# Optimization experiments

Measured on AMD Instinct MI355X. Metric: run time of the kernel, lower is better.

The kernel has to match this reference:

```python
import jax, jax.numpy as jnp
import numpy as np

# --- static module config (from init_kwargs) ---
C1_OUT = 64          # c1OutChannels
C1K = 400            # k winners in conv layer
N_FC = 1024          # fc1 hidden units (n)
K_FC = 100           # k winners in fc1
BOOST = 1.0          # boostStrength
W_SPARSITY = 0.5     # weightSparsity: fraction of fc1 weights allowed nonzero
HP = 12              # pooled spatial size: floor((28-5+1)/2)
C1_OUTPUT_LEN = C1_OUT * HP * HP  # 9216
BATCH = 4096


def setup_inputs() -> dict:
    key = jax.random.key(0)
    ks = jax.random.split(key, 10)
    x = jax.random.normal(ks[0], (BATCH, 1, 28, 28), jnp.float32)
    c1_w = jax.random.normal(ks[1], (C1_OUT, 1, 5, 5), jnp.float32) * 0.1
    c1_b = jax.random.normal(ks[2], (C1_OUT,), jnp.float32) * 0.01
    # duty cycles live in [0, ~density]
    duty_cnn = jax.random.uniform(ks[3], (1, C1_OUT, 1, 1), jnp.float32) * 0.05
    fc1_w = jax.random.normal(ks[4], (N_FC, C1_OUT_LEN_ := C1_OUTPUT_LEN), jnp.float32) * 0.01
    fc1_mask_raw = jax.random.uniform(ks[5], (N_FC, C1_OUTPUT_LEN), jnp.float32)
    fc1_b = jax.random.normal(ks[6], (N_FC,), jnp.float32) * 0.01
    duty_fc = jax.random.uniform(ks[7], (N_FC,), jnp.float32) * 0.1
    fc2_w = jax.random.normal(ks[8], (10, N_FC), jnp.float32) * 0.05
    fc2_b = jnp.zeros((10,), jnp.float32)
    return dict(x=x, c1_w=c1_w, c1_b=c1_b, duty_cnn=duty_cnn, fc1_w=fc1_w,
                fc1_mask_raw=fc1_mask_raw, fc1_b=fc1_b, duty_fc=duty_fc,
                fc2_w=fc2_w, fc2_b=fc2_b)


def _kwinners(x_flat, boost_flat, k):
    """Duty-cycle-boosted k-winner mask.
    x_flat: [B, N]; boost_flat: [1, N] broadcastable boost factors.
    Keeps original x values at the top-k boosted positions per row, zeros rest.
    Boosting uses stop_gradient(x), matching KWinners*.forward(x.detach()*boost).
    """
    boosted = jax.lax.stop_gradient(x_flat) * boost_flat
    thr = jax.lax.top_k(boosted, k)[0][:, -1:]  # k-th largest per row
    return jnp.where(boosted >= thr, x_flat, jnp.zeros((), x_flat.dtype))


def reference(x, c1_w, c1_b, duty_cnn, fc1_w, fc1_mask_raw, fc1_b, duty_fc,
              fc2_w, fc2_b):
    B = x.shape[0]
    # conv2d (valid, stride 1) -> [B, 64, 24, 24]
    y = jax.lax.conv_general_dilated(
        x, c1_w, window_strides=(1, 1), padding='VALID',
        dimension_numbers=('NCHW', 'OIHW', 'NCHW')) + c1_b[None, :, None, None]
    # max_pool2d(2) -> [B, 64, 12, 12]
    y = jax.lax.reduce_window(y, -jnp.inf, jax.lax.max,
                              (1, 1, 2, 2), (1, 1, 2, 2), 'VALID')
    # KWinnersCNN: global top-k over flattened (C,H,W), per-channel boost
    target_density = C1K / C1_OUTPUT_LEN
    boost_c = jnp.exp((target_density - duty_cnn) * BOOST)  # [1,C,1,1]
    boost_flat = jnp.broadcast_to(boost_c, (1, C1_OUT, HP, HP)).reshape(1, -1)
    yf = _kwinners(y.reshape(B, -1), boost_flat, C1K)  # [B, 9216]
    # LinearSDR fc1: sparse-weight linear + KWinners
    w_mask = (fc1_mask_raw < W_SPARSITY).astype(fc1_w.dtype)
    h = yf @ (fc1_w * w_mask).T + fc1_b  # [B, 1024]
    boost_fc = jnp.exp((K_FC / N_FC - duty_fc) * BOOST)[None, :]
    h = _kwinners(h, boost_fc, K_FC)
    # fc2 + log_softmax (dropout inactive in eval mode)
    logits = h @ fc2_w.T + fc2_b
    return jax.nn.log_softmax(logits, axis=1)
```

## Files before the change

kernel.cpp:

```cpp
#include <hip/hip_runtime.h>

__device__ __forceinline__ float b2f(unsigned short u) {
  return __uint_as_float(((unsigned)u) << 16);
}
__device__ __forceinline__ unsigned short f2b(float f) {
  unsigned u = __float_as_uint(f);
  return (unsigned short)((u + 0x7FFFu + ((u >> 16) & 1u)) >> 16);
}
__device__ __forceinline__ float gload(const void* p, int i, int isb) {
  return isb ? b2f(((const unsigned short*)p)[i]) : ((const float*)p)[i];
}
__device__ __forceinline__ unsigned tokey(float f) {
  unsigned u = __float_as_uint(f);
  return u ^ (unsigned)(((int)u >> 31) | 0x80000000u);
}

__global__ void k_detect(const void* x, int* flag) {
  int tid = threadIdx.x;
  unsigned short u = ((const unsigned short*)x)[2 * tid];
  int e = (u >> 7) & 0xFF;
  bool sane = (e >= 100 && e <= 140);
  unsigned long long m = __ballot(sane);
  if (tid == 0) *flag = (__popcll(m) >= 40) ? 1 : 0;
}

__global__ __launch_bounds__(256) void k_prep(const void* __restrict__ fc1w,
                                              const void* __restrict__ mraw,
                                              float* __restrict__ WtF,
                                              const int* __restrict__ flag) {
  __shared__ float tile[64][65];
  const int isb = *flag;
  const int i0 = blockIdx.x * 64;
  const int u0 = blockIdx.y * 64;
  const int tx = threadIdx.x & 63, ty = threadIdx.x >> 6;
  for (int uu = ty; uu < 64; uu += 4) {
    int gi = (u0 + uu) * 9216 + i0 + tx;
    float wv = gload(fc1w, gi, isb);
    float mv = gload(mraw, gi, isb);
    tile[uu][tx] = (mv < 0.5f) ? wv : 0.0f;
  }
  __syncthreads();
  for (int ii = ty; ii < 64; ii += 4)
    WtF[(i0 + ii) * 1024 + u0 + tx] = tile[tx][ii];
}

__global__ __launch_bounds__(256) void k_conv(const void* __restrict__ x,
                                              const void* __restrict__ c1w_g,
                                              const void* __restrict__ c1b_g,
                                              const void* __restrict__ duty_g,
                                              int2* __restrict__ wpair,
                                              int* __restrict__ wcnt,
                                              const int* __restrict__ flag) {
  __shared__ __align__(16) float img[784];
  __shared__ float cw[1600];
  __shared__ float cb[64], bcs[64];
  __shared__ __align__(16) float pooled[9216];
  __shared__ unsigned hist[256];
  __shared__ unsigned selb, selk;
  const int tid = threadIdx.x;
  const int b = blockIdx.x;
  const int isb = *flag;

  for (int i = tid; i < 784; i += 256) img[i] = gload(x, b * 784 + i, isb);
  for (int i = tid; i < 1600; i += 256) cw[i] = gload(c1w_g, i, isb);
  if (tid < 64) {
    cb[tid] = gload(c1b_g, tid, isb);
    float arg = (float)(400.0 / 9216.0) - gload(duty_g, tid, isb);
    bcs[tid] = (float)exp((double)arg);
  }
  __syncthreads();

  for (int s = 0; s < 6; ++s) {
    int t = tid + (s << 8);
    int c = t / 24;
    int sub = t - c * 24;
    int ph = sub >> 1;
    int half = sub & 1;
    float w[25];
#pragma unroll
    for (int i = 0; i < 25; ++i) w[i] = cw[c * 25 + i];
    float R[6][16];
#pragma unroll
    for (int rr = 0; rr < 6; ++rr) {
      int row = 2 * ph + rr;
#pragma unroll
      for (int q = 0; q < 4; ++q)
        ((float4*)&R[rr][0])[q] = ((const float4*)img)[row * 7 + half * 3 + q];
    }
    float a0[12], a1[12];
#pragma unroll
    for (int j = 0; j < 12; ++j) { a0[j] = 0.f; a1[j] = 0.f; }
#pragma unroll
    for (int kj = 0; kj < 5; ++kj) {
#pragma unroll
      for (int kr = 0; kr < 5; ++kr) {
        float wk = w[kr * 5 + kj];
#pragma unroll
        for (int j = 0; j < 12; ++j) {
          a0[j] = fmaf(R[kr][j + kj], wk, a0[j]);
          a1[j] = fmaf(R[kr + 1][j + kj], wk, a1[j]);
        }
      }
    }
    float bias = cb[c];
    int obase = c * 144 + ph * 12 + half * 6;
#pragma unroll
    for (int q = 0; q < 6; ++q) {
      float m = fmaxf(fmaxf(a0[2 * q], a0[2 * q + 1]),
                      fmaxf(a1[2 * q], a1[2 * q + 1]));
      pooled[obase + q] = m + bias;
    }
  }
  __syncthreads();

  unsigned kfix = 0;
  int kk = 400;
  for (int pass = 3; pass >= 0; --pass) {
    const int shift = pass * 8;
    const unsigned himask = (pass == 3) ? 0u : (0xFFFFFFFFu << (shift + 8));
    hist[tid] = 0;
    __syncthreads();
    for (int e = 0; e < 9; ++e) {
      float4 pv = ((float4*)pooled)[tid * 9 + e];
#pragma unroll
      for (int q = 0; q < 4; ++q) {
        int o = tid * 36 + e * 4 + q;
        unsigned key = tokey(((float*)&pv)[q] * bcs[o / 144]);
        if (((key ^ kfix) & himask) == 0)
          atomicAdd(&hist[(key >> shift) & 255u], 1u);
      }
    }
    __syncthreads();
    unsigned v = hist[tid];
    for (int offs = 1; offs < 256; offs <<= 1) {
      unsigned other = (tid + offs < 256) ? hist[tid + offs] : 0u;
      __syncthreads();
      v += other;
      hist[tid] = v;
      __syncthreads();
    }
    unsigned snext = (tid < 255) ? hist[tid + 1] : 0u;
    if (v >= (unsigned)kk && snext < (unsigned)kk) {
      selb = (unsigned)tid;
      selk = (unsigned)(kk - (int)snext);
    }
    __syncthreads();
    kfix |= selb << shift;
    kk = (int)selk;
    __syncthreads();
  }

  int mycnt = 0;
#pragma unroll
  for (int e = 0; e < 36; ++e) {
    int o = tid * 36 + e;
    if (tokey(pooled[o] * bcs[o / 144]) >= kfix) ++mycnt;
  }
  hist[tid] = (unsigned)mycnt;
  __syncthreads();
  unsigned v2 = hist[tid];
  for (int offs = 1; offs < 256; offs <<= 1) {
    unsigned other = (tid >= offs) ? hist[tid - offs] : 0u;
    __syncthreads();
    v2 += other;
    hist[tid] = v2;
    __syncthreads();
  }
  int pos = (int)v2 - mycnt;
  for (int e = 0; e < 36; ++e) {
    int o = tid * 36 + e;
    float pv = pooled[o];
    if (tokey(pv * bcs[o / 144]) >= kfix) {
      if (pos < 512) wpair[b * 512 + pos] = make_int2(__float_as_int(pv), o);
      ++pos;
    }
  }
  if (tid == 255) wcnt[b] = (int)(v2 < 512u ? v2 : 512u);
}

__global__ __launch_bounds__(128) void k_fc1(const float* __restrict__ WtF,
                                             const int2* __restrict__ wpair,
                                             const int* __restrict__ wcnt,
                                             const void* __restrict__ fc1b,
                                             float* __restrict__ h,
                                             const int* __restrict__ flag) {
  __shared__ float sval[512];
  __shared__ int sidx[512];
  const int tid = threadIdx.x;
  const int img = blockIdx.x >> 3;
  const int slice = blockIdx.x & 7;
  const int isb = *flag;
  const int cnt = wcnt[img];
  for (int i = tid; i < cnt; i += 128) {
    int2 p = wpair[img * 512 + i];
    sval[i] = __int_as_float(p.x);
    sidx[i] = p.y;
  }
  __syncthreads();
  const int u = (slice << 7) | tid;
  const float* W = WtF + u;
  float acc = 0.f;
  for (int w = 0; w < cnt; ++w)
    acc = fmaf(sval[w], W[sidx[w] * 1024], acc);
  h[img * 1024 + u] = acc + gload(fc1b, u, isb);
}

__global__ __launch_bounds__(256) void k_sel(const float* __restrict__ h,
                                             const void* __restrict__ dutyfc,
                                             const void* __restrict__ fc2w,
                                             const void* __restrict__ fc2b,
                                             void* __restrict__ out,
                                             const int* __restrict__ flag) {
  __shared__ unsigned hist[256];
  __shared__ unsigned selb, selk;
  __shared__ double lg[10];
  __shared__ double mred[2];
  const int tid = threadIdx.x;
  const int row = blockIdx.x;
  const int isb = *flag;
  if (tid < 10) lg[tid] = (double)gload(fc2b, tid, isb);
  __syncthreads();

  const int u0 = 2 * tid, u1 = 2 * tid + 1, u2 = 512 + 2 * tid, u3 = 513 + 2 * tid;
  float2 hlo = ((const float2*)(h + row * 1024))[tid];
  float2 hhi = ((const float2*)(h + row * 1024 + 512))[tid];
  float h0 = hlo.x, h1 = hlo.y, h2 = hhi.x, h3 = hhi.y;
  float bf0 = (float)exp((double)(0.09765625f - gload(dutyfc, u0, isb)));
  float bf1 = (float)exp((double)(0.09765625f - gload(dutyfc, u1, isb)));
  float bf2 = (float)exp((double)(0.09765625f - gload(dutyfc, u2, isb)));
  float bf3 = (float)exp((double)(0.09765625f - gload(dutyfc, u3, isb)));
  unsigned k0 = tokey(h0 * bf0);
  unsigned k1 = tokey(h1 * bf1);
  unsigned k2 = tokey(h2 * bf2);
  unsigned k3 = tokey(h3 * bf3);

  unsigned kfix = 0;
  int kk = 100;
  for (int pass = 3; pass >= 0; --pass) {
    const int shift = pass * 8;
    const unsigned himask = (pass == 3) ? 0u : (0xFFFFFFFFu << (shift + 8));
    hist[tid] = 0;
    __syncthreads();
    if (((k0 ^ kfix) & himask) == 0) atomicAdd(&hist[(k0 >> shift) & 255u], 1u);
    if (((k1 ^ kfix) & himask) == 0) atomicAdd(&hist[(k1 >> shift) & 255u], 1u);
    if (((k2 ^ kfix) & himask) == 0) atomicAdd(&hist[(k2 >> shift) & 255u], 1u);
    if (((k3 ^ kfix) & himask) == 0) atomicAdd(&hist[(k3 >> shift) & 255u], 1u);
    __syncthreads();
    unsigned v = hist[tid];
    for (int offs = 1; offs < 256; offs <<= 1) {
      unsigned other = (tid + offs < 256) ? hist[tid + offs] : 0u;
      __syncthreads();
      v += other;
      hist[tid] = v;
      __syncthreads();
    }
    unsigned snext = (tid < 255) ? hist[tid + 1] : 0u;
    if (v >= (unsigned)kk && snext < (unsigned)kk) {
      selb = (unsigned)tid;
      selk = (unsigned)(kk - (int)snext);
    }
    __syncthreads();
    kfix |= selb << shift;
    kk = (int)selk;
    __syncthreads();
  }
  bool kp0 = k0 >= kfix, kp1 = k1 >= kfix, kp2 = k2 >= kfix, kp3 = k3 >= kfix;

  double part[10];
#pragma unroll
  for (int c = 0; c < 10; ++c) part[c] = 0.0;
  if (kp0) {
#pragma unroll
    for (int c = 0; c < 10; ++c) part[c] = fma((double)h0, (double)gload(fc2w, c * 1024 + u0, isb), part[c]);
  }
  if (kp1) {
#pragma unroll
    for (int c = 0; c < 10; ++c) part[c] = fma((double)h1, (double)gload(fc2w, c * 1024 + u1, isb), part[c]);
  }
  if (kp2) {
#pragma unroll
    for (int c = 0; c < 10; ++c) part[c] = fma((double)h2, (double)gload(fc2w, c * 1024 + u2, isb), part[c]);
  }
  if (kp3) {
#pragma unroll
    for (int c = 0; c < 10; ++c) part[c] = fma((double)h3, (double)gload(fc2w, c * 1024 + u3, isb), part[c]);
  }
#pragma unroll
  for (int c = 0; c < 10; ++c) {
    double p = part[c];
    for (int off = 32; off > 0; off >>= 1) p += __shfl_xor(p, off);
    if ((tid & 63) == 0) atomicAdd(&lg[c], p);
  }
  __syncthreads();
  if (tid == 0) {
    double m = lg[0];
#pragma unroll
    for (int c = 1; c < 10; ++c) m = lg[c] > m ? lg[c] : m;
    double sum = 0.0;
#pragma unroll
    for (int c = 0; c < 10; ++c) sum += exp(lg[c] - m);
    mred[0] = m;
    mred[1] = log(sum);
  }
  __syncthreads();
  if (tid < 10) {
    double o = lg[tid] - mred[0] - mred[1];
    if (isb)
      ((unsigned short*)out)[row * 10 + tid] = f2b((float)o);
    else
      ((float*)out)[row * 10 + tid] = (float)o;
  }
}

extern "C" void kernel_launch(void* const* d_in, const int* in_sizes, int n_in,
                              void* d_out, int out_size, void* d_ws, size_t ws_size,
                              hipStream_t stream) {
  char* ws = (char*)d_ws;
  float* WtF = (float*)ws;
  int2* wpair = (int2*)(ws + 37748736);
  int* wcnt = (int*)(ws + 54525952);
  float* h = (float*)(ws + 54542336);
  int* flag = (int*)(ws + 71319552);

  k_detect<<<1, 64, 0, stream>>>(d_in[0], flag);
  k_prep<<<dim3(144, 16), 256, 0, stream>>>(d_in[4], d_in[5], WtF, flag);
  k_conv<<<4096, 256, 0, stream>>>(d_in[0], d_in[1], d_in[2], d_in[3],
                                   wpair, wcnt, flag);
  k_fc1<<<4096 * 8, 128, 0, stream>>>(WtF, wpair, wcnt, d_in[6], h, flag);
  k_sel<<<4096, 256, 0, stream>>>(h, d_in[7], d_in[8], d_in[9], d_out, flag);
}
```

Before: 657.0 us.

## Restructure conv with sliding row window, register keys, wave-shuffle scans, float2 fc1

The conv stage now gives each thread one channel quarter with six pooled rows, reusing a rotating register window of input rows instead of reloading six rows per output row. Boosted sort keys are computed once into registers and reused across all radix passes and the final compaction. The shared-memory Hillis-Steele scans are replaced with wavefront shuffle scans plus a small cross-wave total, which cuts many block barriers. fc1 drops the shared staging of winners, broadcasts each pair via readfirstlane, and computes two outputs per thread with float2 loads in 64-thread blocks. The cost is higher register pressure from the 36-key array and the R window, which may reduce occupancy.

```diff
diff --git a/kernel.cpp b/kernel.cpp
--- a/kernel.cpp
+++ b/kernel.cpp
@@ -56,10 +56,13 @@
   __shared__ float cb[64], bcs[64];
   __shared__ __align__(16) float pooled[9216];
   __shared__ unsigned hist[256];
+  __shared__ unsigned wtot[4];
   __shared__ unsigned selb, selk;
   const int tid = threadIdx.x;
   const int b = blockIdx.x;
   const int isb = *flag;
+  const int lane = tid & 63;
+  const int wv_id = tid >> 6;
 
   for (int i = tid; i < 784; i += 256) img[i] = gload(x, b * 784 + i, isb);
   for (int i = tid; i < 1600; i += 256) cw[i] = gload(c1w_g, i, isb);
@@ -70,139 +73,169 @@
   }
   __syncthreads();
 
-  for (int s = 0; s < 6; ++s) {
-    int t = tid + (s << 8);
-    int c = t / 24;
-    int sub = t - c * 24;
-    int ph = sub >> 1;
-    int half = sub & 1;
+  {
+    const int c = tid >> 2;
+    const int half = tid & 1;
+    const int ph0 = ((tid >> 1) & 1) * 6;
     float w[25];
 #pragma unroll
     for (int i = 0; i < 25; ++i) w[i] = cw[c * 25 + i];
+    const float bias = cb[c];
     float R[6][16];
 #pragma unroll
-    for (int rr = 0; rr < 6; ++rr) {
-      int row = 2 * ph + rr;
+    for (int r = 0; r < 6; ++r) {
+      int ir = 2 * ph0 + r;
 #pragma unroll
       for (int q = 0; q < 4; ++q)
-        ((float4*)&R[rr][0])[q] = ((const float4*)img)[row * 7 + half * 3 + q];
-    }
-    float a0[12], a1[12];
-#pragma unroll
-    for (int j = 0; j < 12; ++j) { a0[j] = 0.f; a1[j] = 0.f; }
-#pragma unroll
-    for (int kj = 0; kj < 5; ++kj) {
-#pragma unroll
-      for (int kr = 0; kr < 5; ++kr) {
-        float wk = w[kr * 5 + kj];
-#pragma unroll
-        for (int j = 0; j < 12; ++j) {
-          a0[j] = fmaf(R[kr][j + kj], wk, a0[j]);
-          a1[j] = fmaf(R[kr + 1][j + kj], wk, a1[j]);
+        ((float4*)&R[r][0])[q] = ((const float4*)img)[ir * 7 + half * 3 + q];
+    }
+#pragma unroll
+    for (int i = 0; i < 6; ++i) {
+      const int ph = ph0 + i;
+      float a0[12], a1[12];
+#pragma unroll
+      for (int j = 0; j < 12; ++j) { a0[j] = 0.f; a1[j] = 0.f; }
+#pragma unroll
+      for (int kj = 0; kj < 5; ++kj) {
+#pragma unroll
+        for (int kr = 0; kr < 5; ++kr) {
+          float wk = w[kr * 5 + kj];
+          const float* r0 = &R[(2 * i + kr) % 6][0];
+          const float* r1 = &R[(2 * i + kr + 1) % 6][0];
+#pragma unroll
+          for (int j = 0; j < 12; ++j) {
+            a0[j] = fmaf(r0[j + kj], wk, a0[j]);
+            a1[j] = fmaf(r1[j + kj], wk, a1[j]);
+          }
         }
       }
-    }
-    float bias = cb[c];
-    int obase = c * 144 + ph * 12 + half * 6;
-#pragma unroll
-    for (int q = 0; q < 6; ++q) {
-      float m = fmaxf(fmaxf(a0[2 * q], a0[2 * q + 1]),
-                      fmaxf(a1[2 * q], a1[2 * q + 1]));
-      pooled[obase + q] = m + bias;
-    }
-  }
-  __syncthreads();
+      int obase = c * 144 + ph * 12 + half * 6;
+#pragma unroll
+      for (int q = 0; q < 6; ++q) {
+        float m = fmaxf(fmaxf(a0[2 * q], a0[2 * q + 1]),
+                        fmaxf(a1[2 * q], a1[2 * q + 1]));
+        pooled[obase + q] = m + bias;
+      }
+      if (i < 5) {
+        int ir0 = 2 * ph + 6, ir1 = 2 * ph + 7;
+        float* d0 = &R[(2 * i) % 6][0];
+        float* d1 = &R[(2 * i + 1) % 6][0];
+#pragma unroll
+        for (int q = 0; q < 4; ++q) {
+          ((float4*)d0)[q] = ((const float4*)img)[ir0 * 7 + half * 3 + q];
+          ((float4*)d1)[q] = ((const float4*)img)[ir1 * 7 + half * 3 + q];
+        }
+      }
+    }
+  }
+  __syncthreads();
+
+  unsigned keys[36];
+  {
+    const float bcf = bcs[tid >> 2];
+#pragma unroll
+    for (int e4 = 0; e4 < 9; ++e4) {
+      float4 pv = ((float4*)pooled)[tid * 9 + e4];
+      keys[4 * e4 + 0] = tokey(pv.x * bcf);
+      keys[4 * e4 + 1] = tokey(pv.y * bcf);
+      keys[4 * e4 + 2] = tokey(pv.z * bcf);
+      keys[4 * e4 + 3] = tokey(pv.w * bcf);
+    }
+  }
 
   unsigned kfix = 0;
-  int kk = 400;
+  unsigned kk = 400;
   for (int pass = 3; pass >= 0; --pass) {
     const int shift = pass * 8;
     const unsigned himask = (pass == 3) ? 0u : (0xFFFFFFFFu << (shift + 8));
     hist[tid] = 0;
     __syncthreads();
-    for (int e = 0; e < 9; ++e) {
-      float4 pv = ((float4*)pooled)[tid * 9 + e];
-#pragma unroll
-      for (int q = 0; q < 4; ++q) {
-        int o = tid * 36 + e * 4 + q;
-        unsigned key = tokey(((float*)&pv)[q] * bcs[o / 144]);
-        if (((key ^ kfix) & himask) == 0)
-          atomicAdd(&hist[(key >> shift) & 255u], 1u);
-      }
-    }
-    __syncthreads();
-    unsigned v = hist[tid];
-    for (int offs = 1; offs < 256; offs <<= 1) {
-      unsigned other = (tid + offs < 256) ? hist[tid + offs] : 0u;
-      __syncthreads();
-      v += other;
-      hist[tid] = v;
-      __syncthreads();
-    }
-    unsigned snext = (tid < 255) ? hist[tid + 1] : 0u;
-    if (v >= (unsigned)kk && snext < (unsigned)kk) {
+#pragma unroll
+    for (int e = 0; e < 36; ++e) {
+      unsigned key = keys[e];
+      if (((key ^ kfix) & himask) == 0)
+        atomicAdd(&hist[(key >> shift) & 255u], 1u);
+    }
+    __syncthreads();
+    unsigned own = hist[tid];
+    unsigned v = own;
+#pragma unroll
+    for (int off = 1; off < 64; off <<= 1) {
+      unsigned y = __shfl_down(v, off, 64);
+      if (lane + off < 64) v += y;
+    }
+    if (lane == 0) wtot[wv_id] = v;
+    __syncthreads();
+#pragma unroll
+    for (int w2 = 0; w2 < 4; ++w2)
+      if (w2 > wv_id) v += wtot[w2];
+    unsigned snext = v - own;
+    if (v >= kk && snext < kk) {
       selb = (unsigned)tid;
-      selk = (unsigned)(kk - (int)snext);
+      selk = kk - snext;
     }
     __syncthreads();
     kfix |= selb << shift;
-    kk = (int)selk;
-    __syncthreads();
-  }
-
-  int mycnt = 0;
-#pragma unroll
+    kk = selk;
+    __syncthreads();
+  }
+
+  unsigned mycnt = 0;
+#pragma unroll
+  for (int e = 0; e < 36; ++e) mycnt += (keys[e] >= kfix) ? 1u : 0u;
+  unsigned px = mycnt;
+#pragma unroll
+  for (int off = 1; off < 64; off <<= 1) {
+    unsigned y = __shfl_up(px, off, 64);
+    if (lane >= off) px += y;
+  }
+  if (lane == 63) wtot[wv_id] = px;
+  __syncthreads();
+  unsigned base = 0;
+#pragma unroll
+  for (int w2 = 0; w2 < 4; ++w2)
+    if (w2 < wv_id) base += wtot[w2];
+  int pos = (int)(base + px - mycnt);
   for (int e = 0; e < 36; ++e) {
-    int o = tid * 36 + e;
-    if (tokey(pooled[o] * bcs[o / 144]) >= kfix) ++mycnt;
-  }
-  hist[tid] = (unsigned)mycnt;
-  __syncthreads();
-  unsigned v2 = hist[tid];
-  for (int offs = 1; offs < 256; offs <<= 1) {
-    unsigned other = (tid >= offs) ? hist[tid - offs] : 0u;
-    __syncthreads();
-    v2 += other;
-    hist[tid] = v2;
-    __syncthreads();
-  }
-  int pos = (int)v2 - mycnt;
-  for (int e = 0; e < 36; ++e) {
-    int o = tid * 36 + e;
-    float pv = pooled[o];
-    if (tokey(pv * bcs[o / 144]) >= kfix) {
-      if (pos < 512) wpair[b * 512 + pos] = make_int2(__float_as_int(pv), o);
+    if (keys[e] >= kfix) {
+      int o = tid * 36 + e;
+      if (pos < 512) wpair[b * 512 + pos] = make_int2(__float_as_int(pooled[o]), o);
       ++pos;
     }
   }
-  if (tid == 255) wcnt[b] = (int)(v2 < 512u ? v2 : 512u);
-}
-
-__global__ __launch_bounds__(128) void k_fc1(const float* __restrict__ WtF,
-                                             const int2* __restrict__ wpair,
-                                             const int* __restrict__ wcnt,
-                                             const void* __restrict__ fc1b,
-                                             float* __restrict__ h,
-                                             const int* __restrict__ flag) {
-  __shared__ float sval[512];
-  __shared__ int sidx[512];
+  if (tid == 0) {
+    unsigned tot = wtot[0] + wtot[1] + wtot[2] + wtot[3];
+    wcnt[b] = (int)(tot < 512u ? tot : 512u);
+  }
+}
+
+__global__ __launch_bounds__(64) void k_fc1(const float* __restrict__ WtF,
+                                            const int2* __restrict__ wpair,
+                                            const int* __restrict__ wcnt,
+                                            const void* __restrict__ fc1b,
+                                            float* __restrict__ h,
+                                            const int* __restrict__ flag) {
   const int tid = threadIdx.x;
   const int img = blockIdx.x >> 3;
   const int slice = blockIdx.x & 7;
   const int isb = *flag;
   const int cnt = wcnt[img];
-  for (int i = tid; i < cnt; i += 128) {
-    int2 p = wpair[img * 512 + i];
-    sval[i] = __int_as_float(p.x);
-    sidx[i] = p.y;
-  }
-  __syncthreads();
-  const int u = (slice << 7) | tid;
-  const float* W = WtF + u;
-  float acc = 0.f;
-  for (int w = 0; w < cnt; ++w)
-    acc = fmaf(sval[w], W[sidx[w] * 1024], acc);
-  h[img * 1024 + u] = acc + gload(fc1b, u, isb);
+  const int u = (slice << 7) + 2 * tid;
+  const float* __restrict__ W = WtF + u;
+  const int2* __restrict__ wp = wpair + img * 512;
+  float acc0 = 0.f, acc1 = 0.f;
+  for (int w = 0; w < cnt; ++w) {
+    int2 p = wp[w];
+    int idx = __builtin_amdgcn_readfirstlane(p.y);
+    float v = __int_as_float(__builtin_amdgcn_readfirstlane(p.x));
+    float2 wv2 = *(const float2*)(W + (size_t)idx * 1024);
+    acc0 = fmaf(v, wv2.x, acc0);
+    acc1 = fmaf(v, wv2.y, acc1);
+  }
+  float2 hb;
+  hb.x = acc0 + gload(fc1b, u, isb);
+  hb.y = acc1 + gload(fc1b, u + 1, isb);
+  *(float2*)(h + img * 1024 + u) = hb;
 }
 
 __global__ __launch_bounds__(256) void k_sel(const float* __restrict__ h,
@@ -326,6 +359,6 @@
   k_prep<<<dim3(144, 16), 256, 0, stream>>>(d_in[4], d_in[5], WtF, flag);
   k_conv<<<4096, 256, 0, stream>>>(d_in[0], d_in[1], d_in[2], d_in[3],
                                    wpair, wcnt, flag);
-  k_fc1<<<4096 * 8, 128, 0, stream>>>(WtF, wpair, wcnt, d_in[6], h, flag);
+  k_fc1<<<4096 * 8, 64, 0, stream>>>(WtF, wpair, wcnt, d_in[6], h, flag);
   k_sel<<<4096, 256, 0, stream>>>(h, d_in[7], d_in[8], d_in[9], d_out, flag);
 }
```

Measured after the change: 883.4 us. +34.5%, slower.
